# Kernel optimization log

Measured on AMD Instinct MI355X. Metric: run time of the kernel, lower is better.

## Reference

```python
import jax, jax.numpy as jnp
import numpy as np

N_POI = 100000   # number of POIs
N_EDGE = 50000   # directed hyperedges
N_USER = 50000   # user hyperedges (multi-view)
NNZ = 1_000_000  # nonzeros per incidence matrix
D = 128          # embedding dim
L = 3            # num_layers


def spmm(rows, cols, vals, x, num_rows):
    """COO sparse @ dense: y[r] += vals * x[c]."""
    return jax.ops.segment_sum(vals[:, None] * x[cols], rows, num_segments=num_rows)


def hyper_net(pois, rows1, cols1, vals1, n1, rows2, cols2, vals2, n2, attn):
    """Chained two-hop sparse propagation with relu + residual, layer-attention fusion.
    Dropout omitted (eval mode / deterministic reference)."""
    embs = [pois]
    x = pois
    for _ in range(L):
        m = spmm(rows1, cols1, vals1, x, n1)      # [n1, D] aggregate to hyperedges/users
        m = spmm(rows2, cols2, vals2, m, n2)      # [N_POI, D] propagate back to POIs
        x = jax.nn.relu(m) + embs[-1]             # relu + residual
        embs.append(x)
    w = jax.nn.softmax(attn)                      # [L+1]
    return jnp.einsum('l,lnd->nd', w, jnp.stack(embs))


def setup_inputs() -> dict:
    key = jax.random.key(0)
    ks = jax.random.split(key, 16)
    inp = {
        'pois_embs': jax.random.normal(ks[0], (N_POI, D), dtype=jnp.float32),
        'tar_rows': jax.random.randint(ks[1], (NNZ,), 0, N_EDGE, dtype=jnp.int32),
        'tar_cols': jax.random.randint(ks[2], (NNZ,), 0, N_POI, dtype=jnp.int32),
        'tar_vals': jax.random.uniform(ks[3], (NNZ,), dtype=jnp.float32),
        'src_rows': jax.random.randint(ks[4], (NNZ,), 0, N_POI, dtype=jnp.int32),
        'src_cols': jax.random.randint(ks[5], (NNZ,), 0, N_EDGE, dtype=jnp.int32),
        'src_vals': jax.random.uniform(ks[6], (NNZ,), dtype=jnp.float32),
        'up_rows': jax.random.randint(ks[7], (NNZ,), 0, N_USER, dtype=jnp.int32),
        'up_cols': jax.random.randint(ks[8], (NNZ,), 0, N_POI, dtype=jnp.int32),
        'up_vals': jax.random.uniform(ks[9], (NNZ,), dtype=jnp.float32),
        'pu_rows': jax.random.randint(ks[10], (NNZ,), 0, N_POI, dtype=jnp.int32),
        'pu_cols': jax.random.randint(ks[11], (NNZ,), 0, N_USER, dtype=jnp.int32),
        'pu_vals': jax.random.uniform(ks[12], (NNZ,), dtype=jnp.float32),
        'attn_di': jnp.ones((L + 1,), dtype=jnp.float32),
        'attn_mv': jnp.ones((L + 1,), dtype=jnp.float32),
    }
    return inp


def reference(pois_embs, tar_rows, tar_cols, tar_vals, src_rows, src_cols, src_vals,
              up_rows, up_cols, up_vals, pu_rows, pu_cols, pu_vals, attn_di, attn_mv):
    # Directed hypergraph branch: msg_tar = HG_poi_tar @ x ; msg_src = HG_poi_src @ msg_tar
    di = hyper_net(pois_embs, tar_rows, tar_cols, tar_vals, N_EDGE,
                   src_rows, src_cols, src_vals, N_POI, attn_di)
    # Multi-view (user) hypergraph branch: HG_up @ x ; HG_pu @ msg
    mv = hyper_net(pois_embs, up_rows, up_cols, up_vals, N_USER,
                   pu_rows, pu_cols, pu_vals, N_POI, attn_mv)
    return di + mv
```

## Files before the change

### kernel.cpp

```cpp
#include <hip/hip_runtime.h>

#define NNZC   1000000
#define NPOI   100000
#define NEDGE  50000
#define NUSER  50000
#define DIM    128
#define NL     3

#define PB     64
#define NBKT   196
#define SCANN  (4 * NBKT * PB)

static inline int ceil_div(int a, int b) { return (a + b - 1) / b; }

typedef unsigned int uint32;

__device__ __forceinline__ float bfLO(uint32 u) { return __uint_as_float(u << 16); }
__device__ __forceinline__ float bfHI(uint32 u) { return __uint_as_float(u & 0xffff0000u); }
__device__ __forceinline__ uint32 bf16_rne(float f) {
    uint32 u = __float_as_uint(f);
    return (u + 0x7fffu + ((u >> 16) & 1u)) >> 16;
}
__device__ __forceinline__ uint32 bfPACK(float a, float b) {
    return bf16_rne(a) | (bf16_rne(b) << 16);
}
__device__ __forceinline__ uint32 csrPACK(int col, float val) {
    return ((uint32)col) | (bf16_rne(val) << 17);
}
__device__ __forceinline__ int   csrCOL(uint32 e) { return (int)(e & 0x1FFFFu); }
__device__ __forceinline__ float csrVAL(uint32 e) { return __uint_as_float((e >> 17) << 16); }

__device__ __constant__ const int c_nrows[4]  = { NEDGE, NPOI, NUSER, NPOI };
__device__ __constant__ const int c_cntoff[4] = { 0, NEDGE, NEDGE + NPOI, NEDGE + NPOI + NUSER };
__device__ __constant__ const int c_cap[4]    = { 64, 48, 64, 48 };
__device__ __constant__ const int c_shift[4]  = { 8, 9, 8, 9 };
__device__ __constant__ const long long c_elloff[4] = { 0, 3200000, 8000000, 11200000 };


__global__ __launch_bounds__(1024) void histH_kernel(
    const int* __restrict__ r0, const int* __restrict__ r1,
    const int* __restrict__ r2, const int* __restrict__ r3,
    int* __restrict__ histG) {
    __shared__ int h[NBKT];
    int m = blockIdx.y, p = blockIdx.x;
    for (int i = threadIdx.x; i < NBKT; i += 1024) h[i] = 0;
    __syncthreads();
    const int* r = (m == 0) ? r0 : (m == 1) ? r1 : (m == 2) ? r2 : r3;
    int shift = c_shift[m];
    int lo = (int)(((long long)NNZC * p) >> 6);
    int hi = (int)(((long long)NNZC * (p + 1)) >> 6);
    for (int i = lo + (int)threadIdx.x; i < hi; i += 1024)
        atomicAdd(&h[r[i] >> shift], 1);
    __syncthreads();
    for (int b = threadIdx.x; b < NBKT; b += 1024)
        histG[(m * NBKT + b) * PB + p] = h[b];
}

__global__ __launch_bounds__(256) void scan_kernel(int* __restrict__ g) {
    __shared__ int base[257];
    int t = threadIdx.x;
    const int chunk = SCANN / 256;
    int lo = t * chunk;
    int s = 0;
    for (int i = 0; i < chunk; i++) s += g[lo + i];
    base[t + 1] = s;
    __syncthreads();
    if (t == 0) {
        base[0] = 0;
        for (int i = 1; i <= 256; i++) base[i] += base[i - 1];
    }
    __syncthreads();
    int off = base[t];
    for (int i = 0; i < chunk; i++) { int v = g[lo + i]; g[lo + i] = off; off += v; }
    if (t == 255) g[SCANN] = base[256];
}

__global__ __launch_bounds__(1024) void scatS_kernel(
    const int* __restrict__ r0, const int* __restrict__ r1,
    const int* __restrict__ r2, const int* __restrict__ r3,
    const int* __restrict__ c0, const int* __restrict__ c1,
    const int* __restrict__ c2, const int* __restrict__ c3,
    const float* __restrict__ v0, const float* __restrict__ v1,
    const float* __restrict__ v2, const float* __restrict__ v3,
    const int* __restrict__ scanG, uint2* __restrict__ rec) {
    __shared__ int cur[NBKT];
    int m = blockIdx.y, p = blockIdx.x;
    for (int b = threadIdx.x; b < NBKT; b += 1024)
        cur[b] = scanG[(m * NBKT + b) * PB + p];
    __syncthreads();
    const int*   r = (m == 0) ? r0 : (m == 1) ? r1 : (m == 2) ? r2 : r3;
    const int*   c = (m == 0) ? c0 : (m == 1) ? c1 : (m == 2) ? c2 : c3;
    const float* v = (m == 0) ? v0 : (m == 1) ? v1 : (m == 2) ? v2 : v3;
    int shift = c_shift[m];
    int lo = (int)(((long long)NNZC * p) >> 6);
    int hi = (int)(((long long)NNZC * (p + 1)) >> 6);
    for (int i = lo + (int)threadIdx.x; i < hi; i += 1024) {
        int row = r[i];
        int pos = atomicAdd(&cur[row >> shift], 1);
        rec[pos] = make_uint2((uint32)row, csrPACK(c[i], v[i]));
    }
}

__global__ __launch_bounds__(512) void fillB_kernel(
    const int* __restrict__ scanG, const uint2* __restrict__ rec,
    int* __restrict__ counts_all, uint32* __restrict__ ell) {
    __shared__ int cnt[512];
    int bx = (int)blockIdx.x;
    int m = bx / NBKT, b = bx - m * NBKT;
    int shift = c_shift[m];
    int rowlo = b << shift;
    int bklen = 1 << shift;
    for (int i = threadIdx.x; i < bklen; i += 512) cnt[i] = 0;
    __syncthreads();
    int lo = scanG[(m * NBKT + b) * PB];
    int hi = scanG[(m * NBKT + b + 1) * PB];
    int cap = c_cap[m];
    uint32* ebase = ell + c_elloff[m];
    for (int i = lo + (int)threadIdx.x; i < hi; i += 512) {
        uint2 e = rec[i];
        int row = (int)e.x;
        int pos = atomicAdd(&cnt[row - rowlo], 1);
        ebase[(size_t)row * cap + pos] = e.y;
    }
    __syncthreads();
    int nrows_b = c_nrows[m] - rowlo;
    if (nrows_b > bklen) nrows_b = bklen;
    int* counts = counts_all + c_cntoff[m];
    for (int i = threadIdx.x; i < nrows_b; i += 512)
        counts[rowlo + i] = cnt[i];
}

__global__ void softmax4_kernel(const float* __restrict__ adi,
                                const float* __restrict__ amv,
                                float* __restrict__ w) {
    if (blockIdx.x == 0 && threadIdx.x == 0) {
        for (int b = 0; b < 2; b++) {
            const float* a = b ? amv : adi;
            float m = a[0];
            for (int l = 1; l < 4; l++) m = fmaxf(m, a[l]);
            float e[4]; float s = 0.f;
            for (int l = 0; l < 4; l++) { e[l] = __expf(a[l] - m); s += e[l]; }
            for (int l = 0; l < 4; l++) w[b * 4 + l] = e[l] / s;
        }
    }
}

__global__ void cast_bf16_kernel(const float* __restrict__ src, uint32* __restrict__ dst, int npairs) {
    int i = blockIdx.x * blockDim.x + threadIdx.x;
    if (i < npairs) {
        float2 f = *(const float2*)(src + (size_t)i * 2);
        dst[i] = bfPACK(f.x, f.y);
    }
}

__device__ __forceinline__ void fma8(float2& a0, float2& a1, float2& a2, float2& a3,
                                     float v, uint4 u) {
    a0.x = fmaf(v, bfLO(u.x), a0.x); a0.y = fmaf(v, bfHI(u.x), a0.y);
    a1.x = fmaf(v, bfLO(u.y), a1.x); a1.y = fmaf(v, bfHI(u.y), a1.y);
    a2.x = fmaf(v, bfLO(u.z), a2.x); a2.y = fmaf(v, bfHI(u.z), a2.y);
    a3.x = fmaf(v, bfLO(u.w), a3.x); a3.y = fmaf(v, bfHI(u.w), a3.y);
}

template<int CAP>
__global__ __launch_bounds__(256) void spmm1_kernel(
    const int* __restrict__ counts, const uint32* __restrict__ ell,
    const uint32* __restrict__ xbf, uint32* __restrict__ ybf, int n_rows) {
    int row = (int)((blockIdx.x * blockDim.x + threadIdx.x) >> 4);
    int t   = (int)(threadIdx.x & 15);
    if (row >= n_rows) return;
    int cnt = counts[row];
    const uint32* erow = ell + (size_t)row * CAP;
    float2 a0 = {0.f,0.f}, a1 = {0.f,0.f}, a2 = {0.f,0.f}, a3 = {0.f,0.f};
    int j = 0;
    for (; j + 8 <= cnt; j += 8) {
        uint4 qa = *(const uint4*)(erow + j);
        uint4 qb = *(const uint4*)(erow + j + 4);
        uint4 u0 = *((const uint4*)(xbf + (size_t)csrCOL(qa.x) * 64) + t);
        uint4 u1 = *((const uint4*)(xbf + (size_t)csrCOL(qa.y) * 64) + t);
        uint4 u2 = *((const uint4*)(xbf + (size_t)csrCOL(qa.z) * 64) + t);
        uint4 u3 = *((const uint4*)(xbf + (size_t)csrCOL(qa.w) * 64) + t);
        uint4 u4 = *((const uint4*)(xbf + (size_t)csrCOL(qb.x) * 64) + t);
        uint4 u5 = *((const uint4*)(xbf + (size_t)csrCOL(qb.y) * 64) + t);
        uint4 u6 = *((const uint4*)(xbf + (size_t)csrCOL(qb.z) * 64) + t);
        uint4 u7 = *((const uint4*)(xbf + (size_t)csrCOL(qb.w) * 64) + t);
        fma8(a0,a1,a2,a3, csrVAL(qa.x), u0); fma8(a0,a1,a2,a3, csrVAL(qa.y), u1);
        fma8(a0,a1,a2,a3, csrVAL(qa.z), u2); fma8(a0,a1,a2,a3, csrVAL(qa.w), u3);
        fma8(a0,a1,a2,a3, csrVAL(qb.x), u4); fma8(a0,a1,a2,a3, csrVAL(qb.y), u5);
        fma8(a0,a1,a2,a3, csrVAL(qb.z), u6); fma8(a0,a1,a2,a3, csrVAL(qb.w), u7);
    }
    for (; j + 4 <= cnt; j += 4) {
        uint4 q = *(const uint4*)(erow + j);
        uint4 u0 = *((const uint4*)(xbf + (size_t)csrCOL(q.x) * 64) + t);
        uint4 u1 = *((const uint4*)(xbf + (size_t)csrCOL(q.y) * 64) + t);
        uint4 u2 = *((const uint4*)(xbf + (size_t)csrCOL(q.z) * 64) + t);
        uint4 u3 = *((const uint4*)(xbf + (size_t)csrCOL(q.w) * 64) + t);
        fma8(a0,a1,a2,a3, csrVAL(q.x), u0); fma8(a0,a1,a2,a3, csrVAL(q.y), u1);
        fma8(a0,a1,a2,a3, csrVAL(q.z), u2); fma8(a0,a1,a2,a3, csrVAL(q.w), u3);
    }
    for (; j < cnt; j++) {
        uint32 e = erow[j];
        uint4 u = *((const uint4*)(xbf + (size_t)csrCOL(e) * 64) + t);
        fma8(a0,a1,a2,a3, csrVAL(e), u);
    }
    uint4 o;
    o.x = bfPACK(a0.x, a0.y); o.y = bfPACK(a1.x, a1.y);
    o.z = bfPACK(a2.x, a2.y); o.w = bfPACK(a3.x, a3.y);
    *((uint4*)(ybf + (size_t)row * 64) + t) = o;
}

template<int CAP>
__global__ __launch_bounds__(256) void spmm2_kernel(
    const int* __restrict__ counts, const uint32* __restrict__ ell,
    const uint32* __restrict__ mbf, const uint32* __restrict__ xinbf,
    uint32* __restrict__ xoutbf, int n_rows) {
    int row = (int)((blockIdx.x * blockDim.x + threadIdx.x) >> 4);
    int t   = (int)(threadIdx.x & 15);
    if (row >= n_rows) return;
    int cnt = counts[row];
    const uint32* erow = ell + (size_t)row * CAP;
    float2 a0 = {0.f,0.f}, a1 = {0.f,0.f}, a2 = {0.f,0.f}, a3 = {0.f,0.f};
    int j = 0;
    for (; j + 8 <= cnt; j += 8) {
        uint4 qa = *(const uint4*)(erow + j);
        uint4 qb = *(const uint4*)(erow + j + 4);
        uint4 u0 = *((const uint4*)(mbf + (size_t)csrCOL(qa.x) * 64) + t);
        uint4 u1 = *((const uint4*)(mbf + (size_t)csrCOL(qa.y) * 64) + t);
        uint4 u2 = *((const uint4*)(mbf + (size_t)csrCOL(qa.z) * 64) + t);
        uint4 u3 = *((const uint4*)(mbf + (size_t)csrCOL(qa.w) * 64) + t);
        uint4 u4 = *((const uint4*)(mbf + (size_t)csrCOL(qb.x) * 64) + t);
        uint4 u5 = *((const uint4*)(mbf + (size_t)csrCOL(qb.y) * 64) + t);
        uint4 u6 = *((const uint4*)(mbf + (size_t)csrCOL(qb.z) * 64) + t);
        uint4 u7 = *((const uint4*)(mbf + (size_t)csrCOL(qb.w) * 64) + t);
        fma8(a0,a1,a2,a3, csrVAL(qa.x), u0); fma8(a0,a1,a2,a3, csrVAL(qa.y), u1);
        fma8(a0,a1,a2,a3, csrVAL(qa.z), u2); fma8(a0,a1,a2,a3, csrVAL(qa.w), u3);
        fma8(a0,a1,a2,a3, csrVAL(qb.x), u4); fma8(a0,a1,a2,a3, csrVAL(qb.y), u5);
        fma8(a0,a1,a2,a3, csrVAL(qb.z), u6); fma8(a0,a1,a2,a3, csrVAL(qb.w), u7);
    }
    for (; j + 4 <= cnt; j += 4) {
        uint4 q = *(const uint4*)(erow + j);
        uint4 u0 = *((const uint4*)(mbf + (size_t)csrCOL(q.x) * 64) + t);
        uint4 u1 = *((const uint4*)(mbf + (size_t)csrCOL(q.y) * 64) + t);
        uint4 u2 = *((const uint4*)(mbf + (size_t)csrCOL(q.z) * 64) + t);
        uint4 u3 = *((const uint4*)(mbf + (size_t)csrCOL(q.w) * 64) + t);
        fma8(a0,a1,a2,a3, csrVAL(q.x), u0); fma8(a0,a1,a2,a3, csrVAL(q.y), u1);
        fma8(a0,a1,a2,a3, csrVAL(q.z), u2); fma8(a0,a1,a2,a3, csrVAL(q.w), u3);
    }
    for (; j < cnt; j++) {
        uint32 e = erow[j];
        uint4 u = *((const uint4*)(mbf + (size_t)csrCOL(e) * 64) + t);
        fma8(a0,a1,a2,a3, csrVAL(e), u);
    }
    uint4 ui = *((const uint4*)(xinbf + (size_t)row * 64) + t);
    uint4 o;
    o.x = bfPACK(fmaxf(a0.x, 0.f) + bfLO(ui.x), fmaxf(a0.y, 0.f) + bfHI(ui.x));
    o.y = bfPACK(fmaxf(a1.x, 0.f) + bfLO(ui.y), fmaxf(a1.y, 0.f) + bfHI(ui.y));
    o.z = bfPACK(fmaxf(a2.x, 0.f) + bfLO(ui.z), fmaxf(a2.y, 0.f) + bfHI(ui.z));
    o.w = bfPACK(fmaxf(a3.x, 0.f) + bfLO(ui.w), fmaxf(a3.y, 0.f) + bfHI(ui.w));
    *((uint4*)(xoutbf + (size_t)row * 64) + t) = o;
}

__global__ void epi1_kernel(const float* __restrict__ pois,
                            const uint32* __restrict__ x1, const uint32* __restrict__ x2,
                            const uint32* __restrict__ x3, const float* __restrict__ w,
                            float* __restrict__ out) {
    int i = blockIdx.x * blockDim.x + threadIdx.x;
    if (i < NPOI * 64) {
        float w0 = w[0] + w[4];
        float2 pf = ((const float2*)pois)[i];
        uint32 u1 = x1[i], u2 = x2[i], u3 = x3[i];
        float o0 = w0 * pf.x + w[1] * bfLO(u1) + w[2] * bfLO(u2) + w[3] * bfLO(u3);
        float o1 = w0 * pf.y + w[1] * bfHI(u1) + w[2] * bfHI(u2) + w[3] * bfHI(u3);
        ((float2*)out)[i] = make_float2(o0, o1);
    }
}

__global__ void epi2_kernel(const uint32* __restrict__ x1, const uint32* __restrict__ x2,
                            const uint32* __restrict__ x3, const float* __restrict__ w,
                            float* __restrict__ out) {
    int i = blockIdx.x * blockDim.x + threadIdx.x;
    if (i < NPOI * 64) {
        uint32 u1 = x1[i], u2 = x2[i], u3 = x3[i];
        float2 ov = ((float2*)out)[i];
        ov.x += w[5] * bfLO(u1) + w[6] * bfLO(u2) + w[7] * bfLO(u3);
        ov.y += w[5] * bfHI(u1) + w[6] * bfHI(u2) + w[7] * bfHI(u3);
        ((float2*)out)[i] = ov;
    }
}

extern "C" void kernel_launch(void* const* d_in, const int* in_sizes, int n_in,
                              void* d_out, int out_size, void* d_ws, size_t ws_size,
                              hipStream_t stream) {
    const float* pois = (const float*)d_in[0];
    const int*   rows_in[4] = { (const int*)d_in[1], (const int*)d_in[4],
                                (const int*)d_in[7], (const int*)d_in[10] };
    const int*   cols_in[4] = { (const int*)d_in[2], (const int*)d_in[5],
                                (const int*)d_in[8], (const int*)d_in[11] };
    const float* vals_in[4] = { (const float*)d_in[3], (const float*)d_in[6],
                                (const float*)d_in[9], (const float*)d_in[12] };
    const float* attn_di = (const float*)d_in[13];
    const float* attn_mv = (const float*)d_in[14];
    float* out = (float*)d_out;

    const int NTOT = NEDGE + NPOI + NUSER + NPOI;
    const int cnt_off[4] = { 0, NEDGE, NEDGE + NPOI, NEDGE + NPOI + NUSER };
    const long long ell_off[4] = { 0, 3200000, 8000000, 11200000 };

    char* p = (char*)d_ws;
    float*  wsoft      = (float*)p;  p += 256;
    int*    counts_all = (int*)p;    p += (size_t)NTOT * 4;
    p = (char*)(((size_t)p + 255) & ~255ull);
    int*    scanG      = (int*)p;    p += (size_t)(SCANN + 64) * 4;
    p = (char*)(((size_t)p + 255) & ~255ull);
    uint32* ell        = (uint32*)p; p += (size_t)16000000 * 4;
    uint32* mbf        = (uint32*)p; p += (size_t)NEDGE * 64 * 4;
    uint32* poisbf     = (uint32*)p; p += (size_t)NPOI * 64 * 4;
    uint32* xl[3];
    for (int l = 0; l < 3; l++) { xl[l] = (uint32*)p; p += (size_t)NPOI * 64 * 4; }
    uint2* rec = (uint2*)xl[0];
    (void)ws_size; (void)out_size; (void)n_in; (void)in_sizes;

    histH_kernel<<<dim3(PB, 4), 1024, 0, stream>>>(
        rows_in[0], rows_in[1], rows_in[2], rows_in[3], scanG);
    scan_kernel<<<1, 256, 0, stream>>>(scanG);
    scatS_kernel<<<dim3(PB, 4), 1024, 0, stream>>>(
        rows_in[0], rows_in[1], rows_in[2], rows_in[3],
        cols_in[0], cols_in[1], cols_in[2], cols_in[3],
        vals_in[0], vals_in[1], vals_in[2], vals_in[3],
        scanG, rec);
    fillB_kernel<<<4 * NBKT, 512, 0, stream>>>(scanG, rec, counts_all, ell);

    softmax4_kernel<<<1, 64, 0, stream>>>(attn_di, attn_mv, wsoft);
    cast_bf16_kernel<<<ceil_div(NPOI * 64, 256), 256, 0, stream>>>(pois, poisbf, NPOI * 64);

    for (int br = 0; br < 2; br++) {
        int m1i = br ? 2 : 0;
        int m2i = br ? 3 : 1;
        const int* cn1 = counts_all + cnt_off[m1i];
        const int* cn2 = counts_all + cnt_off[m2i];
        const uint32* el1 = ell + ell_off[m1i];
        const uint32* el2 = ell + ell_off[m2i];
        const int n1 = 50000;
        const uint32* xcur = poisbf;
        for (int l = 1; l <= NL; l++) {
            spmm1_kernel<64><<<ceil_div(n1, 16), 256, 0, stream>>>(cn1, el1, xcur, mbf, n1);
            spmm2_kernel<48><<<ceil_div(NPOI, 16), 256, 0, stream>>>(
                cn2, el2, mbf, xcur, xl[l - 1], NPOI);
            xcur = xl[l - 1];
        }
        if (br == 0)
            epi1_kernel<<<ceil_div(NPOI * 64, 256), 256, 0, stream>>>(
                pois, xl[0], xl[1], xl[2], wsoft, out);
        else
            epi2_kernel<<<ceil_div(NPOI * 64, 256), 256, 0, stream>>>(
                xl[0], xl[1], xl[2], wsoft, out);
    }
}
```

Baseline: 778.0 us.

## Pre-sort COO entries by column bucket before row bucketing for gather locality

Adds a column-bucket counting sort (histogram, scan, scatter) ahead of the existing row-bucket sort. The row pass now reads packed records from the column-sorted intermediate buffer, so each row's entries in the ELL layout come out roughly ordered by column. The intent is that concurrent rows in the SpMM kernels gather from nearby regions of the dense input, improving cache hit rates. The cost is two extra passes over all four incidence matrices and an extra intermediate buffer during preprocessing.

```diff
diff --git a/kernel.cpp b/kernel.cpp
--- a/kernel.cpp
+++ b/kernel.cpp
@@ -10,6 +10,8 @@
 #define PB     64
 #define NBKT   196
 #define SCANN  (4 * NBKT * PB)
+#define NCB    49
+#define SCANC  (4 * NCB * PB)
 
 static inline int ceil_div(int a, int b) { return (a + b - 1) / b; }
 
@@ -34,32 +36,33 @@
 __device__ __constant__ const int c_cntoff[4] = { 0, NEDGE, NEDGE + NPOI, NEDGE + NPOI + NUSER };
 __device__ __constant__ const int c_cap[4]    = { 64, 48, 64, 48 };
 __device__ __constant__ const int c_shift[4]  = { 8, 9, 8, 9 };
+__device__ __constant__ const int c_cshift[4] = { 11, 10, 11, 10 };
 __device__ __constant__ const long long c_elloff[4] = { 0, 3200000, 8000000, 11200000 };
 
 
-__global__ __launch_bounds__(1024) void histH_kernel(
-    const int* __restrict__ r0, const int* __restrict__ r1,
-    const int* __restrict__ r2, const int* __restrict__ r3,
-    int* __restrict__ histG) {
-    __shared__ int h[NBKT];
+__global__ __launch_bounds__(1024) void colHist_kernel(
+    const int* __restrict__ c0, const int* __restrict__ c1,
+    const int* __restrict__ c2, const int* __restrict__ c3,
+    int* __restrict__ histC) {
+    __shared__ int h[NCB];
     int m = blockIdx.y, p = blockIdx.x;
-    for (int i = threadIdx.x; i < NBKT; i += 1024) h[i] = 0;
-    __syncthreads();
-    const int* r = (m == 0) ? r0 : (m == 1) ? r1 : (m == 2) ? r2 : r3;
-    int shift = c_shift[m];
+    for (int i = threadIdx.x; i < NCB; i += 1024) h[i] = 0;
+    __syncthreads();
+    const int* c = (m == 0) ? c0 : (m == 1) ? c1 : (m == 2) ? c2 : c3;
+    int shift = c_cshift[m];
     int lo = (int)(((long long)NNZC * p) >> 6);
     int hi = (int)(((long long)NNZC * (p + 1)) >> 6);
     for (int i = lo + (int)threadIdx.x; i < hi; i += 1024)
-        atomicAdd(&h[r[i] >> shift], 1);
-    __syncthreads();
-    for (int b = threadIdx.x; b < NBKT; b += 1024)
-        histG[(m * NBKT + b) * PB + p] = h[b];
-}
-
-__global__ __launch_bounds__(256) void scan_kernel(int* __restrict__ g) {
+        atomicAdd(&h[c[i] >> shift], 1);
+    __syncthreads();
+    for (int b = threadIdx.x; b < NCB; b += 1024)
+        histC[(m * NCB + b) * PB + p] = h[b];
+}
+
+__global__ __launch_bounds__(256) void scan_kernel(int* __restrict__ g, int n) {
     __shared__ int base[257];
     int t = threadIdx.x;
-    const int chunk = SCANN / 256;
+    int chunk = n >> 8;
     int lo = t * chunk;
     int s = 0;
     for (int i = 0; i < chunk; i++) s += g[lo + i];
@@ -72,32 +75,68 @@
     __syncthreads();
     int off = base[t];
     for (int i = 0; i < chunk; i++) { int v = g[lo + i]; g[lo + i] = off; off += v; }
-    if (t == 255) g[SCANN] = base[256];
-}
-
-__global__ __launch_bounds__(1024) void scatS_kernel(
+    if (t == 255) g[n] = base[256];
+}
+
+__global__ __launch_bounds__(1024) void colScat_kernel(
     const int* __restrict__ r0, const int* __restrict__ r1,
     const int* __restrict__ r2, const int* __restrict__ r3,
     const int* __restrict__ c0, const int* __restrict__ c1,
     const int* __restrict__ c2, const int* __restrict__ c3,
     const float* __restrict__ v0, const float* __restrict__ v1,
     const float* __restrict__ v2, const float* __restrict__ v3,
-    const int* __restrict__ scanG, uint2* __restrict__ rec) {
+    const int* __restrict__ scanC, uint2* __restrict__ rec1) {
+    __shared__ int cur[NCB];
+    int m = blockIdx.y, p = blockIdx.x;
+    for (int b = threadIdx.x; b < NCB; b += 1024)
+        cur[b] = scanC[(m * NCB + b) * PB + p];
+    __syncthreads();
+    const int*   r = (m == 0) ? r0 : (m == 1) ? r1 : (m == 2) ? r2 : r3;
+    const int*   c = (m == 0) ? c0 : (m == 1) ? c1 : (m == 2) ? c2 : c3;
+    const float* v = (m == 0) ? v0 : (m == 1) ? v1 : (m == 2) ? v2 : v3;
+    int shift = c_cshift[m];
+    int lo = (int)(((long long)NNZC * p) >> 6);
+    int hi = (int)(((long long)NNZC * (p + 1)) >> 6);
+    for (int i = lo + (int)threadIdx.x; i < hi; i += 1024) {
+        int col = c[i];
+        int pos = atomicAdd(&cur[col >> shift], 1);
+        rec1[pos] = make_uint2((uint32)r[i], csrPACK(col, v[i]));
+    }
+}
+
+__global__ __launch_bounds__(1024) void histR_kernel(
+    const uint2* __restrict__ rec1, int* __restrict__ histG) {
+    __shared__ int h[NBKT];
+    int m = blockIdx.y, p = blockIdx.x;
+    for (int i = threadIdx.x; i < NBKT; i += 1024) h[i] = 0;
+    __syncthreads();
+    const uint2* rin = rec1 + (size_t)m * NNZC;
+    int shift = c_shift[m];
+    int lo = (int)(((long long)NNZC * p) >> 6);
+    int hi = (int)(((long long)NNZC * (p + 1)) >> 6);
+    for (int i = lo + (int)threadIdx.x; i < hi; i += 1024)
+        atomicAdd(&h[(int)rin[i].x >> shift], 1);
+    __syncthreads();
+    for (int b = threadIdx.x; b < NBKT; b += 1024)
+        histG[(m * NBKT + b) * PB + p] = h[b];
+}
+
+__global__ __launch_bounds__(1024) void scatS_kernel(
+    const uint2* __restrict__ rec1, const int* __restrict__ scanG,
+    uint2* __restrict__ rec2) {
     __shared__ int cur[NBKT];
     int m = blockIdx.y, p = blockIdx.x;
     for (int b = threadIdx.x; b < NBKT; b += 1024)
         cur[b] = scanG[(m * NBKT + b) * PB + p];
     __syncthreads();
-    const int*   r = (m == 0) ? r0 : (m == 1) ? r1 : (m == 2) ? r2 : r3;
-    const int*   c = (m == 0) ? c0 : (m == 1) ? c1 : (m == 2) ? c2 : c3;
-    const float* v = (m == 0) ? v0 : (m == 1) ? v1 : (m == 2) ? v2 : v3;
+    const uint2* rin = rec1 + (size_t)m * NNZC;
     int shift = c_shift[m];
     int lo = (int)(((long long)NNZC * p) >> 6);
     int hi = (int)(((long long)NNZC * (p + 1)) >> 6);
     for (int i = lo + (int)threadIdx.x; i < hi; i += 1024) {
-        int row = r[i];
-        int pos = atomicAdd(&cur[row >> shift], 1);
-        rec[pos] = make_uint2((uint32)row, csrPACK(c[i], v[i]));
+        uint2 e = rin[i];
+        int pos = atomicAdd(&cur[(int)e.x >> shift], 1);
+        rec2[pos] = e;
     }
 }
 
@@ -311,23 +350,29 @@
     p = (char*)(((size_t)p + 255) & ~255ull);
     int*    scanG      = (int*)p;    p += (size_t)(SCANN + 64) * 4;
     p = (char*)(((size_t)p + 255) & ~255ull);
+    int*    scanC      = (int*)p;    p += (size_t)(SCANC + 64) * 4;
+    p = (char*)(((size_t)p + 255) & ~255ull);
     uint32* ell        = (uint32*)p; p += (size_t)16000000 * 4;
     uint32* mbf        = (uint32*)p; p += (size_t)NEDGE * 64 * 4;
     uint32* poisbf     = (uint32*)p; p += (size_t)NPOI * 64 * 4;
     uint32* xl[3];
     for (int l = 0; l < 3; l++) { xl[l] = (uint32*)p; p += (size_t)NPOI * 64 * 4; }
-    uint2* rec = (uint2*)xl[0];
+    uint2* rec1 = (uint2*)xl[0];
+    uint2* rec2 = (uint2*)((char*)xl[0] + (size_t)4 * NNZC * 8);
     (void)ws_size; (void)out_size; (void)n_in; (void)in_sizes;
 
-    histH_kernel<<<dim3(PB, 4), 1024, 0, stream>>>(
-        rows_in[0], rows_in[1], rows_in[2], rows_in[3], scanG);
-    scan_kernel<<<1, 256, 0, stream>>>(scanG);
-    scatS_kernel<<<dim3(PB, 4), 1024, 0, stream>>>(
+    colHist_kernel<<<dim3(PB, 4), 1024, 0, stream>>>(
+        cols_in[0], cols_in[1], cols_in[2], cols_in[3], scanC);
+    scan_kernel<<<1, 256, 0, stream>>>(scanC, SCANC);
+    colScat_kernel<<<dim3(PB, 4), 1024, 0, stream>>>(
         rows_in[0], rows_in[1], rows_in[2], rows_in[3],
         cols_in[0], cols_in[1], cols_in[2], cols_in[3],
         vals_in[0], vals_in[1], vals_in[2], vals_in[3],
-        scanG, rec);
-    fillB_kernel<<<4 * NBKT, 512, 0, stream>>>(scanG, rec, counts_all, ell);
+        scanC, rec1);
+    histR_kernel<<<dim3(PB, 4), 1024, 0, stream>>>(rec1, scanG);
+    scan_kernel<<<1, 256, 0, stream>>>(scanG, SCANN);
+    scatS_kernel<<<dim3(PB, 4), 1024, 0, stream>>>(rec1, scanG, rec2);
+    fillB_kernel<<<4 * NBKT, 512, 0, stream>>>(scanG, rec2, counts_all, ell);
 
     softmax4_kernel<<<1, 64, 0, stream>>>(attn_di, attn_mv, wsoft);
     cast_bf16_kernel<<<ceil_div(NPOI * 64, 256), 256, 0, stream>>>(pois, poisbf, NPOI * 64);
```

After: 870.5 us. +11.9%, slower.
